# Optimization experiments

Hardware: AMD Instinct MI355X
Metric: run time of the kernel (lower is better)

Reference implementation:

```python
import jax, jax.numpy as jnp
import numpy as np
from jax import lax

B, T, L, OUT, SP, E, H = 128, 300, 28, 28, 7, 20, 256
W = T - L + 1          # 273 sliding windows
W_OUT = W - OUT        # 245 training windows
F_IN = L + 1 + E       # 49 rnn input features


def _lstm_dilated(x, d, Wih, Whh, b):
    # x: [T0, B, F]; dilation d realized by phase-stacking time into batch (zalando DRNN scheme)
    T0, Bn, F = x.shape
    pad = (-T0) % d
    if pad:
        x = jnp.concatenate([x, jnp.zeros((pad, Bn, F), x.dtype)], axis=0)
    Tn = x.shape[0] // d
    xd = x.reshape(Tn, d * Bn, F)  # element [k, j*Bn:(j+1)*Bn] == x[k*d+j]
    Hh = Whh.shape[1]

    def step(carry, xt):
        h, c = carry
        z = xt @ Wih.T + h @ Whh.T + b
        i, f, g, o = jnp.split(z, 4, axis=-1)  # torch LSTM gate order i,f,g,o
        c = jax.nn.sigmoid(f) * c + jax.nn.sigmoid(i) * jnp.tanh(g)
        h = jax.nn.sigmoid(o) * jnp.tanh(c)
        return (h, c), h

    h0 = jnp.zeros((d * Bn, Hh), x.dtype)
    _, hs = lax.scan(step, (h0, h0), xd)
    return hs.reshape(Tn * d, Bn, Hh)[:T0]


def _forward(train_dataset, val_dataset, alpha_raw, gamma_raw, init_seas,
             input_categories, my_param,
             Wih1, Whh1, b1, Wih2, Whh2, b2, Wih3, Whh3, b3, Wih4, Whh4, b4,
             linear_W, linear_b, score_W, score_b):
    x = train_dataset
    a = jax.nn.sigmoid(alpha_raw)   # [B]
    g = jax.nn.sigmoid(gamma_raw)   # [B]
    S0 = jnp.exp(init_seas)         # [B,7] = seasonalities[0..6]
    s7 = S0[:, 0]                   # seasonalities[7] = exp(init[:,0])
    level0 = x[:, 0] / S0[:, 0]
    buf0 = jnp.concatenate([S0[:, 1:], s7[:, None]], axis=1)  # S[1..7], shift register

    def es_step(carry, xt):
        level, buf = carry
        s = buf[:, 0]
        lvl = a * (xt / s) + (1.0 - a) * level
        s_new = g * (xt / lvl) + (1.0 - g) * s
        buf = jnp.concatenate([buf[:, 1:], s_new[:, None]], axis=1)
        return (lvl, buf), (lvl, s_new)

    _, (lvls, s_news) = lax.scan(es_step, (level0, buf0), x[:, 1:].T)
    levels = jnp.concatenate([level0[None], lvls], axis=0).T        # [B,T]
    S_full = jnp.concatenate([S0, s7[:, None], s_news.T], axis=1)   # [B,T+7]
    # extension: cat(S_full, S_full[:, T : T-7+28])  -> [B, T+28]
    S_ext = jnp.concatenate([S_full, S_full[:, T:T - SP + OUT]], axis=1)

    # input windows (vectorized over all W window positions)
    widx = jnp.arange(W)[:, None] + jnp.arange(L)[None, :]          # [W,L]
    lvl_w = levels[:, L - 1 + jnp.arange(W)]                        # [B,W]
    norm_in = x[:, widx] / S_ext[:, widx] / lvl_w[:, :, None]       # [B,W,L]
    cats = jnp.broadcast_to(input_categories[:, None, :], (B, W, E))
    cat_in = jnp.concatenate([norm_in, cats], axis=2)[jnp.arange(B) % 10]  # original j%10 row pick
    mp = jnp.broadcast_to(my_param.reshape(1, 1, 1), (B, W, 1))
    window_input = jnp.transpose(jnp.concatenate([cat_in, mp], axis=2), (1, 0, 2))  # [W,B,F_IN]

    # output windows
    oidx = (L + jnp.arange(W_OUT))[:, None] + jnp.arange(OUT)[None, :]  # [W_OUT,OUT]
    lvl_o = levels[:, L - 1 + jnp.arange(W_OUT)]                        # [B,W_OUT]
    window_output = jnp.transpose(x[:, oidx] / S_ext[:, oidx] / lvl_o[:, :, None], (1, 0, 2))

    # residual dilated LSTM stack: block1 dilations (1,2); block2 dilations (2,6) + residual
    h1 = _lstm_dilated(window_input, 1, Wih1, Whh1, b1)
    h1 = _lstm_dilated(h1, 2, Wih2, Whh2, b2)
    h2 = _lstm_dilated(h1, 2, Wih3, Whh3, b3)
    h2 = _lstm_dilated(h2, 6, Wih4, Whh4, b4) + h1
    h = jnp.tanh(h2 @ linear_W.T + linear_b)
    rnn_out = h @ score_W.T + score_b                                   # [W,B,OUT]

    # LSTM stack is causal, so running on window_input[:-OUT] equals slicing the full run
    prediction_values = rnn_out[:-OUT]
    actual_values = window_output
    holdout = rnn_out[-1] * S_ext[:, -OUT:] * levels[:, -1:]
    holdout_prediction = holdout * (holdout > 0).astype(holdout.dtype)
    hav = val_dataset
    hav_norm = hav / S_ext[:, -OUT:] / levels[:, -1:]
    return (prediction_values, actual_values, holdout_prediction, rnn_out, hav, hav_norm)


def setup_inputs() -> dict:
    key = jax.random.key(0)
    ks = jax.random.split(key, 24)
    s = float(1.0 / np.sqrt(H))
    u = lambda k, shape: jax.random.uniform(k, shape, jnp.float32, -s, s)
    inp = {
        "train_dataset": jax.random.uniform(ks[0], (B, T), jnp.float32) * 2.0 + 0.5,  # positive sales
        "val_dataset": jax.random.uniform(ks[1], (B, OUT), jnp.float32) * 2.0 + 0.5,
        "alpha_raw": jnp.full((B,), 0.5, jnp.float32),
        "gamma_raw": jnp.full((B,), 0.5, jnp.float32),
        "init_seas": jnp.full((B, SP), 0.5, jnp.float32),
        "input_categories": jnp.full((B, E), 0.001, jnp.float32) + 0.01 * jax.random.normal(ks[2], (B, E), jnp.float32),
        "my_param": jnp.full((1,), 0.001, jnp.float32),
        "Wih1": u(ks[3], (4 * H, F_IN)), "Whh1": u(ks[4], (4 * H, H)), "b1": u(ks[5], (4 * H,)),
        "Wih2": u(ks[6], (4 * H, H)), "Whh2": u(ks[7], (4 * H, H)), "b2": u(ks[8], (4 * H,)),
        "Wih3": u(ks[9], (4 * H, H)), "Whh3": u(ks[10], (4 * H, H)), "b3": u(ks[11], (4 * H,)),
        "Wih4": u(ks[12], (4 * H, H)), "Whh4": u(ks[13], (4 * H, H)), "b4": u(ks[14], (4 * H,)),
        "linear_W": u(ks[15], (H, H)), "linear_b": u(ks[16], (H,)),
        "score_W": u(ks[17], (OUT, H)), "score_b": u(ks[18], (OUT,)),
    }
    return inp


def reference(train_dataset, val_dataset, alpha_raw, gamma_raw, init_seas,
              input_categories, my_param,
              Wih1, Whh1, b1, Wih2, Whh2, b2, Wih3, Whh3, b3, Wih4, Whh4, b4,
              linear_W, linear_b, score_W, score_b):
    return _forward(train_dataset, val_dataset, alpha_raw, gamma_raw, init_seas,
                    input_categories, my_param,
                    Wih1, Whh1, b1, Wih2, Whh2, b2, Wih3, Whh3, b3, Wih4, Whh4, b4,
                    linear_W, linear_b, score_W, score_b)
```

## Files before the change

kernel.cpp:

```cpp
#include <hip/hip_runtime.h>

typedef unsigned short u16;
typedef unsigned int   u32;

static __device__ __forceinline__ float sigf (float x){ return 1.0f/(1.0f+__expf(-x)); }
static __device__ __forceinline__ float tanh_(float x){ return 2.0f/(1.0f+__expf(-2.0f*x)) - 1.0f; }

#define NM 2730
#define N_O0 878080
#define N_O3 978432

static __device__ __forceinline__ int dot4(u32 a, u32 b, int acc){
#if __has_builtin(__builtin_amdgcn_sdot4)
  return __builtin_amdgcn_sdot4((int)a, (int)b, acc, false);
#else
  int s = acc;
  #pragma unroll
  for(int i=0;i<4;i++){
    int av = (int)((signed char)((a >> (8*i)) & 0xffu));
    int bv = (int)((signed char)((b >> (8*i)) & 0xffu));
    s += av*bv;
  }
  return s;
#endif
}

__global__ __launch_bounds__(256) void k_prep(
    const float* __restrict__ x,     float* __restrict__ xT,
    const float* __restrict__ wi0,   float* __restrict__ wT0,
    const float* __restrict__ wi1,   float* __restrict__ wT1,
    const float* __restrict__ wi2,   float* __restrict__ wT2,
    const float* __restrict__ wi3,   float* __restrict__ wT3,
    const float* __restrict__ lw,    float* __restrict__ lwT,
    const float* __restrict__ sw,    float* __restrict__ swT,
    const float* __restrict__ h0, const float* __restrict__ h1,
    const float* __restrict__ h2, const float* __restrict__ h3,
    float* __restrict__ zsc){
  int i = blockIdx.x*256 + threadIdx.x;
  if(i < 38400){
    int t = i >> 7, b = i & 127;
    xT[i] = x[b*300 + t];
    return;
  }
  i -= 38400;
  if(i < 50176){ int c=i/1024, r=i-c*1024; wT0[i] = wi0[r*49 + c];  return; }
  i -= 50176;
  if(i < 262144){ int c=i>>10, r=i&1023; wT1[i] = wi1[r*256 + c];   return; }
  i -= 262144;
  if(i < 262144){ int c=i>>10, r=i&1023; wT2[i] = wi2[r*256 + c];   return; }
  i -= 262144;
  if(i < 262144){ int c=i>>10, r=i&1023; wT3[i] = wi3[r*256 + c];   return; }
  i -= 262144;
  if(i < 65536){ int c=i>>8, r=i&255; lwT[i] = lw[r*256 + c];       return; }
  i -= 65536;
  if(i < 7168){ int c=i/28, r=i-c*28; swT[i] = sw[r*256 + c];       return; }
  i -= 7168;
  if(i < 4096){
    int l = i >> 10, r = i & 1023;
    const float* W = (l==0)?h0:(l==1)?h1:(l==2)?h2:h3;
    const float4* p = (const float4*)(W + (size_t)r*256);
    float m = 0.f;
    #pragma unroll 8
    for(int q=0;q<64;q++){
      float4 v = p[q];
      m = fmaxf(m, fmaxf(fmaxf(fabsf(v.x),fabsf(v.y)), fmaxf(fabsf(v.z),fabsf(v.w))));
    }
    zsc[i] = fmaxf(m, 1e-20f) * (1.0f/16129.0f);
  }
}

__global__ __launch_bounds__(256) void k_packes(
    const float* __restrict__ h0, const float* __restrict__ h1,
    const float* __restrict__ h2, const float* __restrict__ h3,
    const float* __restrict__ zsc, u32* __restrict__ W8,
    const float* __restrict__ xT, const float* __restrict__ alpha,
    const float* __restrict__ gamma, const float* __restrict__ iseas,
    float* __restrict__ ST, float* __restrict__ lvlT){
  if(blockIdx.x < 1024){
    int i = blockIdx.x*256 + threadIdx.x;
    int l = i >> 16;
    int uidx = i & 65535;
    int dw = uidx & 3;
    int kg = (uidx >> 2) & 127;
    int q  = (uidx >> 9) & 3;
    int rr = (uidx >> 11) & 7;
    int js = uidx >> 14;
    int row = rr*128 + kg;
    int k0  = js*64 + q*16 + dw*4;
    const float* W = (l==0)?h0:(l==1)?h1:(l==2)?h2:h3;
    float inv = 1.0f / (zsc[l*1024 + row] * 127.0f);
    u32 out = 0;
    #pragma unroll
    for(int b=0;b<4;b++){
      float v = W[(size_t)row*256 + k0 + b];
      int q8 = max(-127, min(127, __float2int_rn(v * inv)));
      out |= ((u32)(q8 & 0xff)) << (8*b);
    }
    W8[i] = out;
    return;
  }
  int b = threadIdx.x;
  if(b >= 128) return;
  float a = sigf(alpha[b]);
  float g = sigf(gamma[b]);
  float S0[7];
  #pragma unroll
  for(int i=0;i<7;i++){ S0[i] = __expf(iseas[b*7+i]); ST[i*128+b] = S0[i]; }
  ST[7*128+b] = S0[0];
  float q0=S0[1],q1=S0[2],q2=S0[3],q3=S0[4],q4=S0[5],q5=S0[6],q6=S0[0];
  float lvl = xT[b]/S0[0];
  lvlT[b] = lvl;
  for(int t=1;t<300;t++){
    float xt = xT[t*128+b];
    float s  = q0;
    lvl = a*(xt/s) + (1.0f-a)*lvl;
    float sn = g*(xt/lvl) + (1.0f-g)*s;
    q0=q1;q1=q2;q2=q3;q3=q4;q4=q5;q5=q6;q6=sn;
    lvlT[t*128+b]   = lvl;
    ST[(t+7)*128+b] = sn;
  }
}

__global__ __launch_bounds__(256) void k_gemm1(
    const float* __restrict__ xT, const float* __restrict__ ST,
    const float* __restrict__ lvlT, const float* __restrict__ cats,
    const float* __restrict__ mp,
    const float* __restrict__ WT,
    const float* __restrict__ bias,
    float* __restrict__ Z){
  __shared__ float Xs[8][52];
  const int tid = threadIdx.x;
  const int m0 = blockIdx.x*8;
  for(int idx=tid; idx<8*49; idx+=256){
    int p = idx/49, f = idx - p*49;
    int m = m0+p;
    float v = 0.f;
    if(m < NM){
      int tt = m/10, jj = m - (m/10)*10;
      if(f < 28){
        int c = tt + f;
        v = xT[c*128 + jj] / ST[c*128 + jj] / lvlT[(tt+27)*128 + jj];
      } else if(f < 48){
        v = cats[jj*20 + (f-28)];
      } else {
        v = mp[0];
      }
    }
    Xs[p][f] = v;
  }
  __syncthreads();
  float acc0[8], acc1[8], acc2[8], acc3[8];
  {
    float b0 = bias[tid];
    float b1 = bias[tid+256];
    float b2 = bias[tid+512];
    float b3 = bias[tid+768];
    #pragma unroll
    for(int p=0;p<8;p++){ acc0[p]=b0; acc1[p]=b1; acc2[p]=b2; acc3[p]=b3; }
  }
  #pragma unroll 7
  for(int f=0; f<49; f++){
    float w0 = WT[f*1024 + tid      ];
    float w1 = WT[f*1024 + tid+256  ];
    float w2 = WT[f*1024 + tid+512  ];
    float w3 = WT[f*1024 + tid+768  ];
    #pragma unroll
    for(int p=0;p<8;p++){
      float xv = Xs[p][f];
      acc0[p] += w0*xv; acc1[p] += w1*xv; acc2[p] += w2*xv; acc3[p] += w3*xv;
    }
  }
  for(int p=0;p<8;p++){
    int m = m0+p;
    if(m < NM){
      float* zb = Z + m*1024 + tid;
      zb[0]=acc0[p]; zb[256]=acc1[p]; zb[512]=acc2[p]; zb[768]=acc3[p];
    }
  }
}

__global__ __launch_bounds__(256) void k_gemm(const float* __restrict__ X,
                                              const float* __restrict__ WT,
                                              const float* __restrict__ bias,
                                              float* __restrict__ Z){
  __shared__ float Xs[8][256];
  const int tid = threadIdx.x;
  const int m0 = blockIdx.x*8;
  for(int p=0;p<8;p++){
    int m = m0+p;
    Xs[p][tid] = (m < NM) ? X[m*256+tid] : 0.0f;
  }
  __syncthreads();
  float acc0[8], acc1[8], acc2[8], acc3[8];
  {
    float b0 = bias[tid];
    float b1 = bias[tid+256];
    float b2 = bias[tid+512];
    float b3 = bias[tid+768];
    #pragma unroll
    for(int p=0;p<8;p++){ acc0[p]=b0; acc1[p]=b1; acc2[p]=b2; acc3[p]=b3; }
  }
  #pragma unroll 4
  for(int f=0; f<256; f++){
    float w0 = WT[f*1024 + tid      ];
    float w1 = WT[f*1024 + tid+256  ];
    float w2 = WT[f*1024 + tid+512  ];
    float w3 = WT[f*1024 + tid+768  ];
    #pragma unroll
    for(int p=0;p<8;p++){
      float xv = Xs[p][f];
      acc0[p] += w0*xv; acc1[p] += w1*xv; acc2[p] += w2*xv; acc3[p] += w3*xv;
    }
  }
  for(int p=0;p<8;p++){
    int m = m0+p;
    if(m < NM){
      float* zb = Z + m*1024 + tid;
      zb[0]=acc0[p]; zb[256]=acc1[p]; zb[512]=acc2[p]; zb[768]=acc3[p];
    }
  }
}

__global__ __launch_bounds__(512) void k_scan8(
    const float* __restrict__ Z,
    const u32* __restrict__ W8,
    const float* __restrict__ zsc,
    float* __restrict__ Y,
    const float* __restrict__ RES,
    int d){
  __shared__ __align__(16) u32 h8[64];
  __shared__ int   zp[4][1024];
  __shared__ float sc[1024];
  __shared__ __align__(16) u32 wl[5*2048];
  const int tid = threadIdx.x;
  const int chain = blockIdx.x;
  const int j = chain % 10;
  const int r = chain / 10;
  const int ns = (273 - r + d - 1)/d;
  const int kg = tid & 127;
  const int js = tid >> 7;
  const uint4* Wb = (const uint4*)W8 + (size_t)js*4096 + kg;
  const uint4* hq = (const uint4*)h8 + js*4;
  uint4* wl4 = (uint4*)wl;

  for(int i=tid;i<1024;i+=512) sc[i] = zsc[i];
  #pragma unroll
  for(int rr=0;rr<5;rr++) wl4[rr*512 + tid] = Wb[rr*512];
  if(tid < 64) h8[tid] = 0u;
  float cst = 0.0f;
  __syncthreads();

  int t = r;
  for(int s=0; s<ns; s++, t+=d){
    const size_t row = (size_t)(t*10 + j);
    float zv0=0.f, zv1=0.f, zv2=0.f, zv3=0.f, rv=0.f;
    if(tid < 256){
      const float* zb = Z + row*1024;
      zv0 = zb[tid]; zv1 = zb[tid+256]; zv2 = zb[tid+512]; zv3 = zb[tid+768];
      if(RES) rv = RES[row*256 + tid];
    }
    int a0=0,a1=0,a2=0,a3=0,a4=0,a5=0,a6=0,a7=0;
    #pragma unroll
    for(int q=0;q<4;q++){
      uint4 h4 = hq[q];
      #pragma unroll
      for(int rr=0;rr<8;rr++){
        uint4 w = (q==0 && rr<5) ? wl4[rr*512 + tid] : Wb[rr*512 + q*128];
        int* ap = (rr==0)?&a0:(rr==1)?&a1:(rr==2)?&a2:(rr==3)?&a3:
                  (rr==4)?&a4:(rr==5)?&a5:(rr==6)?&a6:&a7;
        int acc = *ap;
        acc = dot4(w.x, h4.x, acc);
        acc = dot4(w.y, h4.y, acc);
        acc = dot4(w.z, h4.z, acc);
        acc = dot4(w.w, h4.w, acc);
        *ap = acc;
      }
    }
    zp[js][       kg] = a0;
    zp[js][128  + kg] = a1;
    zp[js][256  + kg] = a2;
    zp[js][384  + kg] = a3;
    zp[js][512  + kg] = a4;
    zp[js][640  + kg] = a5;
    zp[js][768  + kg] = a6;
    zp[js][896  + kg] = a7;
    __syncthreads();
    if(tid < 256){
      const int u = tid;
      int si = zp[0][u]     + zp[1][u]     + zp[2][u]     + zp[3][u];
      int sf = zp[0][u+256] + zp[1][u+256] + zp[2][u+256] + zp[3][u+256];
      int sg = zp[0][u+512] + zp[1][u+512] + zp[2][u+512] + zp[3][u+512];
      int so = zp[0][u+768] + zp[1][u+768] + zp[2][u+768] + zp[3][u+768];
      float zi = zv0 + sc[u]     * (float)si;
      float zf = zv1 + sc[u+256] * (float)sf;
      float zg = zv2 + sc[u+512] * (float)sg;
      float zo = zv3 + sc[u+768] * (float)so;
      float c  = sigf(zf)*cst + sigf(zi)*tanh_(zg);
      float h  = sigf(zo)*tanh_(c);
      cst = c;
      int hqi = __float2int_rn(h * 127.0f);
      hqi = max(-127, min(127, hqi));
      ((signed char*)h8)[u] = (signed char)hqi;
      Y[row*256 + u] = h + rv;
    }
    __syncthreads();
  }
}

__global__ __launch_bounds__(256) void k_headout(const float* __restrict__ Y4,
    const float* __restrict__ LWT,
    const float* __restrict__ lb,
    const float* __restrict__ SWT,
    const float* __restrict__ sb,
    const float* __restrict__ ST, const float* __restrict__ lvlT,
    const float* __restrict__ xT, const float* __restrict__ val,
    float* __restrict__ out){
  __shared__ float v [8][256];
  __shared__ float h2[8][256];
  const int tid = threadIdx.x;
  if(blockIdx.x >= 342){
    int i = (blockIdx.x - 342)*256 + tid;
    if(i < N_O0){
      int o = i % 28;
      int b = (i/28) % 128;
      int t = i/(28*128);
      int c = 28 + t + o;
      out[878080 + i] = xT[c*128+b] / ST[c*128+b] / lvlT[(27+t)*128+b];
    } else {
      i -= N_O0;
      if(i < 3584){
        int b = i/28, o = i%28;
        int col = (o < 21) ? (286+o) : (279+o);
        float Sm = ST[col*128 + b];
        float lv = lvlT[299*128 + b];
        out[2738176 + i] = val[i];
        out[2741760 + i] = val[i] / Sm / lv;
      }
    }
    return;
  }
  const int m0 = blockIdx.x*8;
  for(int p=0;p<8;p++){
    int m = m0+p;
    v[p][tid] = (m<NM) ? Y4[m*256+tid] : 0.0f;
  }
  __syncthreads();
  float acc[8];
  float bz = lb[tid];
  #pragma unroll
  for(int p=0;p<8;p++) acc[p]=bz;
  #pragma unroll 4
  for(int f=0; f<256; f++){
    float w = LWT[f*256+tid];
    #pragma unroll
    for(int p=0;p<8;p++) acc[p] += w * v[p][f];
  }
  #pragma unroll
  for(int p=0;p<8;p++) h2[p][tid] = tanh_(acc[p]);
  __syncthreads();
  if(tid < 224){
    int o = tid % 28, p = tid / 28;
    int m = m0 + p;
    if(m < NM){
      float a = sb[o];
      for(int f=0; f<256; f++) a += SWT[f*28+o] * h2[p][f];
      int t = m / 10, j = m - t*10;
      float* o0 = out;
      float* o3 = out + 1759744;
      for(int b=j; b<128; b+=10){
        size_t idx = (size_t)t*3584 + b*28 + o;
        o3[idx] = a;
        if(t < 245) o0[idx] = a;
      }
      if(t == 272){
        int col = (o < 21) ? (286+o) : (279+o);
        float* o2 = out + 1756160;
        for(int b=j; b<128; b+=10){
          float hv = a * ST[col*128 + b] * lvlT[299*128 + b];
          o2[b*28 + o] = (hv > 0.0f) ? hv : 0.0f;
        }
      }
    }
  }
}

extern "C" void kernel_launch(void* const* d_in, const int* in_sizes, int n_in,
                              void* d_out, int out_size, void* d_ws, size_t ws_size,
                              hipStream_t stream){
  (void)in_sizes; (void)n_in; (void)out_size; (void)ws_size;
  const float* x     = (const float*)d_in[0];
  const float* val   = (const float*)d_in[1];
  const float* alpha = (const float*)d_in[2];
  const float* gamma = (const float*)d_in[3];
  const float* iseas = (const float*)d_in[4];
  const float* cats  = (const float*)d_in[5];
  const float* mp    = (const float*)d_in[6];
  const float* Wih[4]  = {(const float*)d_in[7],  (const float*)d_in[10], (const float*)d_in[13], (const float*)d_in[16]};
  const float* Whh[4]  = {(const float*)d_in[8],  (const float*)d_in[11], (const float*)d_in[14], (const float*)d_in[17]};
  const float* bias[4] = {(const float*)d_in[9],  (const float*)d_in[12], (const float*)d_in[15], (const float*)d_in[18]};
  const float* linW  = (const float*)d_in[19];
  const float* linb  = (const float*)d_in[20];
  const float* scW   = (const float*)d_in[21];
  const float* scb   = (const float*)d_in[22];

  float* Fw   = (float*)d_ws;
  float* ST   = Fw;
  float* lvlT = ST   + 39296;
  float* xT   = lvlT + 38400;
  float* xz   = xT   + 38400;
  float* yA   = xz   + 2795520;
  float* yB   = yA   + 698880;
  float* wihT[4];
  wihT[0] = yB + 698880;
  wihT[1] = wihT[0] + 50176;
  wihT[2] = wihT[1] + 262144;
  wihT[3] = wihT[2] + 262144;
  float* linWT = wihT[3] + 262144;
  float* scT   = linWT + 65536;
  float* zsc   = scT   + 7168;
  u32*   W8all = (u32*)(zsc + 4096);

  k_prep<<<3718, 256, 0, stream>>>(x, xT,
      Wih[0], wihT[0], Wih[1], wihT[1], Wih[2], wihT[2], Wih[3], wihT[3],
      linW, linWT, scW, scT,
      Whh[0], Whh[1], Whh[2], Whh[3], zsc);

  k_packes<<<1025, 256, 0, stream>>>(Whh[0], Whh[1], Whh[2], Whh[3], zsc, W8all,
                                     xT, alpha, gamma, iseas, ST, lvlT);

  const int    dlt[4]    = {1, 2, 2, 6};
  const int    chains[4] = {10, 20, 20, 60};
  const float* Xin[4]    = {nullptr, yA, yB, yA};
  float*       Yout[4]   = {yA, yB, yA, yA};
  for(int l=0;l<4;l++){
    if(l == 0)
      k_gemm1<<<(NM+7)/8, 256, 0, stream>>>(xT, ST, lvlT, cats, mp,
                                            wihT[0], bias[0], xz);
    else
      k_gemm<<<(NM+7)/8, 256, 0, stream>>>(Xin[l], wihT[l], bias[l], xz);
    k_scan8<<<chains[l], 512, 0, stream>>>(xz, W8all + l*65536, zsc + l*1024,
                                           Yout[l],
                                           (l==3) ? yB : (const float*)nullptr, dlt[l]);
  }

  k_headout<<<342 + (N_O0 + 3584 + 255)/256, 256, 0, stream>>>(
      yA, linWT, linb, scT, scb, ST, lvlT, xT, val, (float*)d_out);
}
```

Baseline: 1.035 ms.

## Restructure LSTM scan: shuffle-reduced K-split, double-buffered h, larger LDS weight cache

The recurrent scan kernel is rewritten so each group of four adjacent lanes splits the K dimension and reduces with warp shuffles instead of going through shared memory. This removes the zp partial-sum array and one barrier per step. The hidden-state int8 buffer is double-buffered, and up to 13 of the 32 weight chunks are cached in dynamic LDS, requested through hipFuncSetAttribute with a fallback to 7 chunks. The weight packing is re-laid out to match the new thread mapping. More LDS per block lowers occupancy, but there are only a few blocks per layer, so this should matter little.

```diff
diff --git a/kernel.cpp b/kernel.cpp
--- a/kernel.cpp
+++ b/kernel.cpp
@@ -79,12 +79,12 @@
   if(blockIdx.x < 1024){
     int i = blockIdx.x*256 + threadIdx.x;
     int l = i >> 16;
-    int uidx = i & 65535;
-    int dw = uidx & 3;
-    int kg = (uidx >> 2) & 127;
-    int q  = (uidx >> 9) & 3;
-    int rr = (uidx >> 11) & 7;
-    int js = uidx >> 14;
+    int w = i & 65535;
+    int dw  = w & 3;
+    int tid = (w >> 2) & 511;
+    int combo = w >> 11;
+    int kg = tid >> 2, js = tid & 3;
+    int rr = combo >> 2, q = combo & 3;
     int row = rr*128 + kg;
     int k0  = js*64 + q*16 + dw*4;
     const float* W = (l==0)?h0:(l==1)?h1:(l==2)?h2:h3;
@@ -221,87 +221,96 @@
   }
 }
 
-__global__ __launch_bounds__(512) void k_scan8(
+template<int NC>
+__global__ __launch_bounds__(512) void k_scan9(
     const float* __restrict__ Z,
     const u32* __restrict__ W8,
     const float* __restrict__ zsc,
     float* __restrict__ Y,
     const float* __restrict__ RES,
     int d){
-  __shared__ __align__(16) u32 h8[64];
-  __shared__ int   zp[4][1024];
-  __shared__ float sc[1024];
-  __shared__ __align__(16) u32 wl[5*2048];
+  extern __shared__ u32 dyn[];
+  u32* wl = dyn;
+  u32* h8 = dyn + NC*2048;
   const int tid = threadIdx.x;
   const int chain = blockIdx.x;
   const int j = chain % 10;
   const int r = chain / 10;
   const int ns = (273 - r + d - 1)/d;
-  const int kg = tid & 127;
-  const int js = tid >> 7;
-  const uint4* Wb = (const uint4*)W8 + (size_t)js*4096 + kg;
-  const uint4* hq = (const uint4*)h8 + js*4;
-  uint4* wl4 = (uint4*)wl;
-
-  for(int i=tid;i<1024;i+=512) sc[i] = zsc[i];
-  #pragma unroll
-  for(int rr=0;rr<5;rr++) wl4[rr*512 + tid] = Wb[rr*512];
+  const int kg = tid >> 2;
+  const int js = tid & 3;
+  const bool comb = (js == 0);
+  const uint4* Wg = (const uint4*)W8;
+
+  #pragma unroll
+  for(int c=0;c<NC;c++)
+    ((uint4*)wl)[c*512 + tid] = Wg[c*512 + tid];
   if(tid < 64) h8[tid] = 0u;
-  float cst = 0.0f;
+  float scr[8];
+  #pragma unroll
+  for(int rr=0;rr<8;rr++) scr[rr] = zsc[rr*128 + kg];
+  float cst0 = 0.f, cst1 = 0.f;
   __syncthreads();
 
   int t = r;
   for(int s=0; s<ns; s++, t+=d){
     const size_t row = (size_t)(t*10 + j);
-    float zv0=0.f, zv1=0.f, zv2=0.f, zv3=0.f, rv=0.f;
-    if(tid < 256){
+    float zv[8]; float rv0=0.f, rv1=0.f;
+    if(comb){
       const float* zb = Z + row*1024;
-      zv0 = zb[tid]; zv1 = zb[tid+256]; zv2 = zb[tid+512]; zv3 = zb[tid+768];
-      if(RES) rv = RES[row*256 + tid];
-    }
-    int a0=0,a1=0,a2=0,a3=0,a4=0,a5=0,a6=0,a7=0;
-    #pragma unroll
-    for(int q=0;q<4;q++){
-      uint4 h4 = hq[q];
       #pragma unroll
-      for(int rr=0;rr<8;rr++){
-        uint4 w = (q==0 && rr<5) ? wl4[rr*512 + tid] : Wb[rr*512 + q*128];
-        int* ap = (rr==0)?&a0:(rr==1)?&a1:(rr==2)?&a2:(rr==3)?&a3:
-                  (rr==4)?&a4:(rr==5)?&a5:(rr==6)?&a6:&a7;
-        int acc = *ap;
-        acc = dot4(w.x, h4.x, acc);
-        acc = dot4(w.y, h4.y, acc);
-        acc = dot4(w.z, h4.z, acc);
-        acc = dot4(w.w, h4.w, acc);
-        *ap = acc;
+      for(int g=0;g<4;g++){
+        zv[2*g]   = zb[g*256 + kg];
+        zv[2*g+1] = zb[g*256 + 128 + kg];
       }
-    }
-    zp[js][       kg] = a0;
-    zp[js][128  + kg] = a1;
-    zp[js][256  + kg] = a2;
-    zp[js][384  + kg] = a3;
-    zp[js][512  + kg] = a4;
-    zp[js][640  + kg] = a5;
-    zp[js][768  + kg] = a6;
-    zp[js][896  + kg] = a7;
-    __syncthreads();
-    if(tid < 256){
-      const int u = tid;
-      int si = zp[0][u]     + zp[1][u]     + zp[2][u]     + zp[3][u];
-      int sf = zp[0][u+256] + zp[1][u+256] + zp[2][u+256] + zp[3][u+256];
-      int sg = zp[0][u+512] + zp[1][u+512] + zp[2][u+512] + zp[3][u+512];
-      int so = zp[0][u+768] + zp[1][u+768] + zp[2][u+768] + zp[3][u+768];
-      float zi = zv0 + sc[u]     * (float)si;
-      float zf = zv1 + sc[u+256] * (float)sf;
-      float zg = zv2 + sc[u+512] * (float)sg;
-      float zo = zv3 + sc[u+768] * (float)so;
-      float c  = sigf(zf)*cst + sigf(zi)*tanh_(zg);
-      float h  = sigf(zo)*tanh_(c);
-      cst = c;
-      int hqi = __float2int_rn(h * 127.0f);
-      hqi = max(-127, min(127, hqi));
-      ((signed char*)h8)[u] = (signed char)hqi;
-      Y[row*256 + u] = h + rv;
+      if(RES){ rv0 = RES[row*256 + kg]; rv1 = RES[row*256 + 128 + kg]; }
+    }
+    const uint4* hq4 = (const uint4*)(h8 + (s&1)*64);
+    uint4 hq0 = hq4[js*4+0], hq1 = hq4[js*4+1];
+    uint4 hq2 = hq4[js*4+2], hq3 = hq4[js*4+3];
+    int a[8];
+    #pragma unroll
+    for(int rr=0;rr<8;rr++) a[rr]=0;
+    #pragma unroll
+    for(int ci=0; ci<32; ci++){
+      const int c = (ci + NC) & 31;
+      const int rr = c >> 2, q = c & 3;
+      uint4 w = (c < NC) ? ((const uint4*)wl)[c*512 + tid]
+                         : Wg[c*512 + tid];
+      uint4 h4 = (q==0)?hq0:(q==1)?hq1:(q==2)?hq2:hq3;
+      int acc = a[rr];
+      acc = dot4(w.x, h4.x, acc);
+      acc = dot4(w.y, h4.y, acc);
+      acc = dot4(w.z, h4.z, acc);
+      acc = dot4(w.w, h4.w, acc);
+      a[rr] = acc;
+    }
+    #pragma unroll
+    for(int rr=0;rr<8;rr++){
+      a[rr] += __shfl_xor(a[rr], 1);
+      a[rr] += __shfl_xor(a[rr], 2);
+    }
+    if(comb){
+      float zi0 = zv[0] + scr[0]*(float)a[0];
+      float zi1 = zv[1] + scr[1]*(float)a[1];
+      float zf0 = zv[2] + scr[2]*(float)a[2];
+      float zf1 = zv[3] + scr[3]*(float)a[3];
+      float zg0 = zv[4] + scr[4]*(float)a[4];
+      float zg1 = zv[5] + scr[5]*(float)a[5];
+      float zo0 = zv[6] + scr[6]*(float)a[6];
+      float zo1 = zv[7] + scr[7]*(float)a[7];
+      float c0 = sigf(zf0)*cst0 + sigf(zi0)*tanh_(zg0);
+      float h0 = sigf(zo0)*tanh_(c0);
+      float c1 = sigf(zf1)*cst1 + sigf(zi1)*tanh_(zg1);
+      float h1 = sigf(zo1)*tanh_(c1);
+      cst0 = c0; cst1 = c1;
+      int q0 = max(-127, min(127, __float2int_rn(h0*127.f)));
+      int q1 = max(-127, min(127, __float2int_rn(h1*127.f)));
+      signed char* hb = (signed char*)(h8 + ((s+1)&1)*64);
+      hb[kg]       = (signed char)q0;
+      hb[kg + 128] = (signed char)q1;
+      Y[row*256 + kg]       = h0 + rv0;
+      Y[row*256 + 128 + kg] = h1 + rv1;
     }
     __syncthreads();
   }
@@ -420,6 +429,12 @@
   float* zsc   = scT   + 7168;
   u32*   W8all = (u32*)(zsc + 4096);
 
+  const int sm13 = 13*8192 + 512;
+  const int sm7  = 7*8192 + 512;
+  hipError_t ae = hipFuncSetAttribute((const void*)k_scan9<13>,
+                    hipFuncAttributeMaxDynamicSharedMemorySize, sm13);
+  const bool big = (ae == hipSuccess);
+
   k_prep<<<3718, 256, 0, stream>>>(x, xT,
       Wih[0], wihT[0], Wih[1], wihT[1], Wih[2], wihT[2], Wih[3], wihT[3],
       linW, linWT, scW, scT,
@@ -438,9 +453,13 @@
                                             wihT[0], bias[0], xz);
     else
       k_gemm<<<(NM+7)/8, 256, 0, stream>>>(Xin[l], wihT[l], bias[l], xz);
-    k_scan8<<<chains[l], 512, 0, stream>>>(xz, W8all + l*65536, zsc + l*1024,
-                                           Yout[l],
-                                           (l==3) ? yB : (const float*)nullptr, dlt[l]);
+    const float* res = (l==3) ? yB : (const float*)nullptr;
+    if(big)
+      k_scan9<13><<<chains[l], 512, sm13, stream>>>(xz, W8all + l*65536,
+                                        zsc + l*1024, Yout[l], res, dlt[l]);
+    else
+      k_scan9<7><<<chains[l], 512, sm7, stream>>>(xz, W8all + l*65536,
+                                        zsc + l*1024, Yout[l], res, dlt[l]);
   }
 
   k_headout<<<342 + (N_O0 + 3584 + 255)/256, 256, 0, stream>>>(
```

Result: slower. 1.477 ms (+42.8%).
